# Optimization experiments

Measured on AMD Instinct MI355X. Metric: run time of the kernel, lower is better.

The kernel has to match this reference:

```python
import jax, jax.numpy as jnp
import numpy as np

B, T, M, P, N2 = 16, 8192, 128, 128, 128  # N2 = N//2 complex modes

def setup_inputs() -> dict:
    key = jax.random.key(0)
    k1, k2, k3, k4, k5 = jax.random.split(key, 5)
    u = jax.random.normal(k1, (B, T, M), dtype=jnp.float32)
    # log-parametrized Lambda (S5 'log' convention): Lambda = -exp(row0) + 1j*row1
    log_re = jnp.log(jax.random.uniform(k2, (N2,), minval=0.1, maxval=1.0))
    im = jnp.pi * jnp.arange(N2, dtype=jnp.float32)  # HiPPO-like imaginary spread
    Lambda_param = jnp.stack([log_re, im], axis=0).astype(jnp.float32)
    B_param = jax.random.normal(k3, (2, N2, M), dtype=jnp.float32) / np.sqrt(M)
    C_param = jax.random.normal(k4, (2, P, N2), dtype=jnp.float32) / np.sqrt(N2)
    delta = jnp.array([0.01], dtype=jnp.float32)  # default_\u0394
    return {"u": u, "Lambda_param": Lambda_param, "B_param": B_param,
            "C_param": C_param, "delta": delta}

def reference(u, Lambda_param, B_param, C_param, delta):
    # Reconstruct complex continuous-time matrices
    Lam = (-jnp.exp(Lambda_param[0]) + 1j * Lambda_param[1]).astype(jnp.complex64)   # (N2,)
    Bc = (B_param[0] + 1j * B_param[1]).astype(jnp.complex64)                        # (N2, M)
    Cc = (C_param[0] + 1j * C_param[1]).astype(jnp.complex64)                        # (P, N2)
    d = delta[0]
    # ZOH discretization: Lambda_d = exp(Lam*d), Bd = ((Lambda_d - 1)/Lam) * B
    Ld = jnp.exp(Lam * d)                                                            # (N2,)
    Bd = ((Ld - 1.0) / Lam)[:, None] * Bc                                            # (N2, M)
    # Input projection: Bu[b,t,n] = sum_m u[b,t,m] * Bd[n,m]
    Bu = jnp.einsum('btm,nm->btn', u.astype(jnp.complex64), Bd)                      # (B,T,N2)
    # Parallel scan of x_{k+1} = Ld * x_k + Bu_k, x_0 = 0 -> x holds x_1..x_T
    A = jnp.broadcast_to(Ld, Bu.shape)
    def comb(e1, e2):
        a1, b1 = e1
        a2, b2 = e2
        return (a1 * a2, a2 * b1 + b2)
    _, x = jax.lax.associative_scan(comb, (A, Bu), axis=1)                           # (B,T,N2)
    # return_next_y=True: y_k = 2*Re(C x_{k+1})
    y = 2.0 * jnp.real(jnp.einsum('btn,pn->btp', x, Cc))                             # (B,T,P)
    return y
```

## Files before the change

### kernel.cpp

```cpp
#include <hip/hip_runtime.h>
#include <hip/hip_bf16.h>

#define LCH 128
#define NCH 64
#define NCHUNKS 1024

typedef __attribute__((ext_vector_type(8))) short short8v;
typedef __attribute__((ext_vector_type(4))) short short4v;
typedef __attribute__((ext_vector_type(4))) float f32x4;

#define W2_LDINV 0
#define W2_LDP   16384
#define W2_E     32768
#define W2_CIN   163840
#define WS_WPACK_BYTE  (589824 * 4)
#define WS_CCPACK_BYTE (589824 * 4 + 65536)

#define BUS_BYTE(s, np) ((((s) >> 3) * 4096) + ((np) * 16) + (((s) & 7) * 2))

__device__ inline unsigned short f2bf(float f) {
    union { __hip_bfloat16 h; unsigned short u; } v;
    v.h = __float2bfloat16(f);
    return v.u;
}
__device__ inline short4v pack4(float a, float b, float c, float d) {
    union { __hip_bfloat162 h2[2]; short4v s4; } pk;
    pk.h2[0] = __float22bfloat162_rn(make_float2(a, b));
    pk.h2[1] = __float22bfloat162_rn(make_float2(c, d));
    return pk.s4;
}

__global__ void k0_pows(const float* __restrict__ lp, const float* __restrict__ delta,
                        float2* __restrict__ ws2) {
    const int r = blockIdx.x;
    const int tid = threadIdx.x;
    const int n = tid & 127;
    const double d = (double)delta[0];
    const double lre = -exp((double)lp[n]);
    const double lim = (double)lp[128 + n];
    const double kk = (double)(r + 1) * d;
    if (tid < 128) {
        const double mag = exp(-lre * kk);
        ws2[W2_LDINV + r * 128 + n] = make_float2((float)(mag * cos(lim * kk)),
                                                  (float)(-mag * sin(lim * kk)));
    } else {
        const double mag = exp(lre * kk);
        ws2[W2_LDP + r * 128 + n] = make_float2((float)(mag * cos(lim * kk)),
                                                (float)(mag * sin(lim * kk)));
    }
}

__global__ void k0_wpack(const float* __restrict__ lp, const float* __restrict__ bp,
                         const float* __restrict__ delta, unsigned short* __restrict__ wpack) {
    const int gid = blockIdx.x * 512 + threadIdx.x;
    const int j = gid & 7;
    const int lane = (gid >> 3) & 63;
    const int ks = (gid >> 9) & 3;
    const int ntile = gid >> 11;
    const int np = ntile * 16 + (lane & 15);
    const int m = ks * 32 + ((lane >> 4) & 3) * 8 + j;
    const int n = np & 127;
    const double d = (double)delta[0];
    const double lre = -exp((double)lp[n]);
    const double lim = (double)lp[128 + n];
    const double er = exp(lre * d);
    const double ldr = er * cos(lim * d), ldi = er * sin(lim * d);
    const double nr = ldr - 1.0, ni = ldi;
    const double den = lre * lre + lim * lim;
    const double cr = (nr * lre + ni * lim) / den;
    const double ci = (ni * lre - nr * lim) / den;
    const double br = (double)bp[n * 128 + m];
    const double bi = (double)bp[16384 + n * 128 + m];
    const double v = (np < 128) ? (cr * br - ci * bi) : (cr * bi + ci * br);
    wpack[gid] = f2bf((float)v);
}

__global__ void k0_cpack(const float* __restrict__ cp, unsigned short* __restrict__ ccpack) {
    const int gid = blockIdx.x * 512 + threadIdx.x;
    const int j = gid & 7;
    const int lane = (gid >> 3) & 63;
    const int ks = (gid >> 9) & 7;
    const int ptile = gid >> 12;
    const int p = ptile * 16 + (lane & 15);
    const int k = ks * 32 + ((lane >> 4) & 3) * 8 + j;
    const int n = k >> 1;
    const float v = ((k & 1) == 0) ? 2.0f * cp[p * 128 + n] : -2.0f * cp[16384 + p * 128 + n];
    ccpack[gid] = f2bf(v);
}

__device__ inline void stage_u(const float* __restrict__ uchunk, unsigned short* lds_u) {
    const float4* uf = (const float4*)uchunk;
    const int tid = threadIdx.x;
#pragma unroll
    for (int it = 0; it < 8; ++it) {
        const int f4 = it * 512 + tid;
        const float4 v = uf[f4];
        const int t = f4 >> 5;
        const int m = (f4 & 31) * 4;
        const int byte = (t * 256 + m * 2) ^ ((t & 7) << 4);
        *(short4v*)((char*)lds_u + byte) = pack4(v.x, v.y, v.z, v.w);
    }
}

__global__ __launch_bounds__(512, 4) void k1_end(const float* __restrict__ u,
                                                 float2* __restrict__ ws2,
                                                 const unsigned short* __restrict__ wpack) {
    __shared__ unsigned short lds_u[16384];
    const int tid = threadIdx.x;
    const int lane = tid & 63;
    const int w = tid >> 6;
    const int tl = lane & 15;
    const int gq = (lane >> 4) & 3;
    const int g = blockIdx.x;
    const int b = g >> 6;
    const int c = g & 63;
    const int n = w * 16 + tl;
    stage_u(u + (size_t)(b * 8192 + c * 128) * 128, lds_u);
    __syncthreads();
    const short8v* wp = (const short8v*)wpack;
    float er = 0.f, ei = 0.f;
#pragma unroll
    for (int h = 0; h < 2; ++h) {
        f32x4 acc[4][2];
#pragma unroll
        for (int i = 0; i < 4; ++i) { acc[i][0] = (f32x4)0.f; acc[i][1] = (f32x4)0.f; }
        __builtin_amdgcn_s_setprio(1);
#pragma unroll
        for (int ks = 0; ks < 4; ++ks) {
            const short8v b0 = wp[(w * 4 + ks) * 64 + lane];
            const short8v b1 = wp[((8 + w) * 4 + ks) * 64 + lane];
#pragma unroll
            for (int tt2 = 0; tt2 < 4; ++tt2) {
                const int t = (h * 4 + tt2) * 16 + tl;
                const int byte = (t * 256 + (ks * 32 + gq * 8) * 2) ^ ((t & 7) << 4);
                const short8v a = *(const short8v*)((const char*)lds_u + byte);
                acc[tt2][0] = __builtin_amdgcn_mfma_f32_16x16x32_bf16(a, b0, acc[tt2][0], 0, 0, 0);
                acc[tt2][1] = __builtin_amdgcn_mfma_f32_16x16x32_bf16(a, b1, acc[tt2][1], 0, 0, 0);
            }
        }
        __builtin_amdgcn_s_setprio(0);
        __builtin_amdgcn_sched_barrier(0);
#pragma unroll
        for (int tt2 = 0; tt2 < 4; ++tt2) {
#pragma unroll
            for (int reg = 0; reg < 4; ++reg) {
                const int r = (h * 4 + tt2) * 16 + gq * 4 + reg;
                const float2 li = ws2[W2_LDINV + r * 128 + n];
                const float br = acc[tt2][0][reg], bi = acc[tt2][1][reg];
                er += li.x * br - li.y * bi;
                ei += li.x * bi + li.y * br;
            }
        }
        __builtin_amdgcn_sched_barrier(0);
    }
    er += __shfl_xor(er, 16); ei += __shfl_xor(ei, 16);
    er += __shfl_xor(er, 32); ei += __shfl_xor(ei, 32);
    const float2 ld = ws2[W2_LDP + 127 * 128 + n];
    if (lane < 16) {
        ws2[W2_E + g * 128 + n] = make_float2(ld.x * er - ld.y * ei,
                                              ld.x * ei + ld.y * er);
    }
}

__global__ void k2_carry(float2* __restrict__ ws2) {
    const int idx = blockIdx.x * 256 + threadIdx.x;
    const int b = idx >> 7;
    const int n = idx & 127;
    const float2 l = ws2[W2_LDP + 127 * 128 + n];
    float cr = 0.f, ci = 0.f;
    for (int c = 0; c < NCH; ++c) {
        const int o = (b * NCH + c) * 128 + n;
        ws2[W2_CIN + o] = make_float2(cr, ci);
        const float2 e = ws2[W2_E + o];
        const float nr = fmaf(l.x, cr, fmaf(-l.y, ci, e.x));
        const float ni = fmaf(l.x, ci, fmaf(l.y, cr, e.y));
        cr = nr; ci = ni;
    }
}

__global__ __launch_bounds__(512, 4) void k3_main(const float* __restrict__ u,
                                                  const float2* __restrict__ ws2,
                                                  const unsigned short* __restrict__ wpack,
                                                  const unsigned short* __restrict__ ccpack,
                                                  float* __restrict__ y) {
    __shared__ unsigned short lds[32768];
    unsigned short* lds_u = lds;
    const int tid = threadIdx.x;
    const int lane = tid & 63;
    const int w = tid >> 6;
    const int tl = lane & 15;
    const int gq = (lane >> 4) & 3;
    const int g = blockIdx.x;
    const int b = g >> 6;
    const int c = g & 63;
    const int n = w * 16 + tl;

    stage_u(u + (size_t)(b * 8192 + c * 128) * 128, lds_u);
    __syncthreads();

    const short8v* wp = (const short8v*)wpack;
#pragma unroll
    for (int hh = 0; hh < 2; ++hh) {
        const int h = 1 - hh;
        f32x4 acc[4][2];
#pragma unroll
        for (int i = 0; i < 4; ++i) { acc[i][0] = (f32x4)0.f; acc[i][1] = (f32x4)0.f; }
        __builtin_amdgcn_s_setprio(1);
#pragma unroll
        for (int ks = 0; ks < 4; ++ks) {
            const short8v b0 = wp[(w * 4 + ks) * 64 + lane];
            const short8v b1 = wp[((8 + w) * 4 + ks) * 64 + lane];
#pragma unroll
            for (int tt2 = 0; tt2 < 4; ++tt2) {
                const int t = (h * 4 + tt2) * 16 + tl;
                const int byte = (t * 256 + (ks * 32 + gq * 8) * 2) ^ ((t & 7) << 4);
                const short8v a = *(const short8v*)((const char*)lds_u + byte);
                acc[tt2][0] = __builtin_amdgcn_mfma_f32_16x16x32_bf16(a, b0, acc[tt2][0], 0, 0, 0);
                acc[tt2][1] = __builtin_amdgcn_mfma_f32_16x16x32_bf16(a, b1, acc[tt2][1], 0, 0, 0);
            }
        }
        __builtin_amdgcn_s_setprio(0);
        __builtin_amdgcn_sched_barrier(0);
        if (h == 0) __syncthreads();
#pragma unroll
        for (int tt2 = 0; tt2 < 4; ++tt2) {
            float vr[4], vi[4];
#pragma unroll
            for (int reg = 0; reg < 4; ++reg) {
                const int r = (h * 4 + tt2) * 16 + gq * 4 + reg;
                const float2 li = ws2[W2_LDINV + r * 128 + n];
                const float br = acc[tt2][0][reg], bi = acc[tt2][1][reg];
                vr[reg] = li.x * br - li.y * bi;
                vi[reg] = li.x * bi + li.y * br;
            }
            const int s0 = (h * 4 + tt2) * 16 + gq * 4;
            const int rowr = w * 16 + tl;
            const int rowi = 128 + rowr;
            *(short4v*)((char*)lds + BUS_BYTE(s0, rowr)) = pack4(vr[0], vr[1], vr[2], vr[3]);
            *(short4v*)((char*)lds + BUS_BYTE(s0, rowi)) = pack4(vi[0], vi[1], vi[2], vi[3]);
        }
        __builtin_amdgcn_sched_barrier(0);
    }

    short8v ONES, D0, D1;
#pragma unroll
    for (int j = 0; j < 8; ++j) {
        const int sl = gq * 8 + j;
        ONES[j] = (short)0x3F80;
        D0[j] = (sl <= tl) ? (short)0x3F80 : (short)0;
        D1[j] = (sl <= tl + 16) ? (short)0x3F80 : (short)0;
    }
    f32x4 z[8][2];
#pragma unroll
    for (int i = 0; i < 8; ++i) { z[i][0] = (f32x4)0.f; z[i][1] = (f32x4)0.f; }
#pragma unroll
    for (int ks = 0; ks < 4; ++ks) {
        const int sb = ks * 32 + gq * 8;
        const int rowr = w * 16 + tl;
        const int rowi = 128 + rowr;
        const short8v b0 = *(const short8v*)((const char*)lds + BUS_BYTE(sb, rowr));
        const short8v b1 = *(const short8v*)((const char*)lds + BUS_BYTE(sb, rowi));
#pragma unroll
        for (int tt = 0; tt < 8; ++tt) {
            if (tt < 2 * ks) continue;
            const short8v a = (tt == 2 * ks) ? D0 : ((tt == 2 * ks + 1) ? D1 : ONES);
            z[tt][0] = __builtin_amdgcn_mfma_f32_16x16x32_bf16(a, b0, z[tt][0], 0, 0, 0);
            z[tt][1] = __builtin_amdgcn_mfma_f32_16x16x32_bf16(a, b1, z[tt][1], 0, 0, 0);
        }
    }
    __syncthreads();

    const float2 cin = ws2[W2_CIN + g * 128 + n];
#pragma unroll
    for (int tt = 0; tt < 8; ++tt) {
#pragma unroll
        for (int reg = 0; reg < 4; ++reg) {
            const int r = tt * 16 + gq * 4 + reg;
            const float2 ld = ws2[W2_LDP + r * 128 + n];
            const float zr = z[tt][0][reg] + cin.x;
            const float zi = z[tt][1][reg] + cin.y;
            const float xr = ld.x * zr - ld.y * zi;
            const float xi = ld.x * zi + ld.y * zr;
            union { __hip_bfloat162 h2; unsigned uu; } pk;
            pk.h2 = __float22bfloat162_rn(make_float2(xr, xi));
            const int byte = (r * 512 + n * 4) ^ ((r & 7) << 4);
            *(unsigned*)((char*)lds + byte) = pk.uu;
        }
    }
    __syncthreads();

    const short8v* cc = (const short8v*)ccpack;
    f32x4 yac[8];
#pragma unroll
    for (int i = 0; i < 8; ++i) yac[i] = (f32x4)0.f;
    __builtin_amdgcn_s_setprio(1);
#pragma unroll
    for (int ks = 0; ks < 8; ++ks) {
        const short8v bfrg = cc[(w * 8 + ks) * 64 + lane];
#pragma unroll
        for (int tt = 0; tt < 8; ++tt) {
            const int t = tt * 16 + tl;
            const int byte = (t * 512 + (ks * 32 + gq * 8) * 2) ^ ((t & 7) << 4);
            const short8v a = *(const short8v*)((const char*)lds + byte);
            yac[tt] = __builtin_amdgcn_mfma_f32_16x16x32_bf16(a, bfrg, yac[tt], 0, 0, 0);
        }
    }
    __builtin_amdgcn_s_setprio(0);
    const int p = w * 16 + tl;
    float* yrow = y + (size_t)(b * 8192 + c * 128) * 128;
#pragma unroll
    for (int tt = 0; tt < 8; ++tt) {
#pragma unroll
        for (int reg = 0; reg < 4; ++reg) {
            const int t = tt * 16 + gq * 4 + reg;
            yrow[t * 128 + p] = yac[tt][reg];
        }
    }
}

extern "C" void kernel_launch(void* const* d_in, const int* in_sizes, int n_in,
                              void* d_out, int out_size, void* d_ws, size_t ws_size,
                              hipStream_t stream) {
    const float* u     = (const float*)d_in[0];
    const float* lp    = (const float*)d_in[1];
    const float* bp    = (const float*)d_in[2];
    const float* cp    = (const float*)d_in[3];
    const float* delta = (const float*)d_in[4];
    float* y  = (float*)d_out;
    float2* ws2 = (float2*)d_ws;
    unsigned short* wpack  = (unsigned short*)((char*)d_ws + WS_WPACK_BYTE);
    unsigned short* ccpack = (unsigned short*)((char*)d_ws + WS_CCPACK_BYTE);

    k0_pows <<<128, 256, 0, stream>>>(lp, delta, ws2);
    k0_wpack<<<64, 512, 0, stream>>>(lp, bp, delta, wpack);
    k0_cpack<<<64, 512, 0, stream>>>(cp, ccpack);
    k1_end  <<<NCHUNKS, 512, 0, stream>>>(u, ws2, wpack);
    k2_carry<<<8, 256, 0, stream>>>(ws2);
    k3_main <<<NCHUNKS, 512, 0, stream>>>(u, ws2, wpack, ccpack, y);
}
```

Before: 88.36 us.

## Materialize bf16 Bu to global workspace instead of recomputing input projection

The first pass now stores the Lambda-inverse-scaled Bu chunk (bf16, 64KB per chunk) to global workspace while it computes the chunk end-state sums. The final pass reads that buffer back instead of re-staging u and redoing the input-projection MFMAs. This removes a second read of u and a repeat of the projection GEMM, at the cost of writing and reading 64MB of intermediate data. The new path is taken only when the workspace is large enough, otherwise the old three-kernel path runs.

```diff
diff --git a/kernel.cpp b/kernel.cpp
--- a/kernel.cpp
+++ b/kernel.cpp
@@ -13,8 +13,10 @@
 #define W2_LDP   16384
 #define W2_E     32768
 #define W2_CIN   163840
-#define WS_WPACK_BYTE  (589824 * 4)
-#define WS_CCPACK_BYTE (589824 * 4 + 65536)
+#define WS_WPACK_BYTE  2359296
+#define WS_CCPACK_BYTE (2359296 + 65536)
+#define WS_BUS_BYTE    (2359296 + 131072)
+#define WS_NEED ((size_t)WS_BUS_BYTE + (size_t)NCHUNKS * 65536)
 
 #define BUS_BYTE(s, np) ((((s) >> 3) * 4096) + ((np) * 16) + (((s) & 7) * 2))
 
@@ -102,6 +104,185 @@
     }
 }
 
+__global__ __launch_bounds__(512, 6) void k3a_bus(const float* __restrict__ u,
+                                                  float2* __restrict__ ws2,
+                                                  const unsigned short* __restrict__ wpack,
+                                                  char* __restrict__ busg) {
+    __shared__ unsigned short lds_u[16384];
+    const int tid = threadIdx.x;
+    const int lane = tid & 63;
+    const int w = tid >> 6;
+    const int tl = lane & 15;
+    const int gq = (lane >> 4) & 3;
+    const int g = blockIdx.x;
+    const int b = g >> 6;
+    const int c = g & 63;
+    const int n = w * 16 + tl;
+    const short8v* wp = (const short8v*)wpack;
+    char* busc = busg + (size_t)g * 65536;
+
+    stage_u(u + (size_t)(b * 8192 + c * 128) * 128, lds_u);
+    __syncthreads();
+
+    float er = 0.f, ei = 0.f;
+#pragma unroll
+    for (int h = 0; h < 2; ++h) {
+        f32x4 acc[4][2];
+#pragma unroll
+        for (int i = 0; i < 4; ++i) { acc[i][0] = (f32x4)0.f; acc[i][1] = (f32x4)0.f; }
+        __builtin_amdgcn_s_setprio(1);
+#pragma unroll
+        for (int ks = 0; ks < 4; ++ks) {
+            const short8v b0 = wp[(w * 4 + ks) * 64 + lane];
+            const short8v b1 = wp[((8 + w) * 4 + ks) * 64 + lane];
+#pragma unroll
+            for (int tt2 = 0; tt2 < 4; ++tt2) {
+                const int t = (h * 4 + tt2) * 16 + tl;
+                const int byte = (t * 256 + (ks * 32 + gq * 8) * 2) ^ ((t & 7) << 4);
+                const short8v a = *(const short8v*)((const char*)lds_u + byte);
+                acc[tt2][0] = __builtin_amdgcn_mfma_f32_16x16x32_bf16(a, b0, acc[tt2][0], 0, 0, 0);
+                acc[tt2][1] = __builtin_amdgcn_mfma_f32_16x16x32_bf16(a, b1, acc[tt2][1], 0, 0, 0);
+            }
+        }
+        __builtin_amdgcn_s_setprio(0);
+        __builtin_amdgcn_sched_barrier(0);
+#pragma unroll
+        for (int tt2 = 0; tt2 < 4; ++tt2) {
+            float vr[4], vi[4];
+#pragma unroll
+            for (int reg = 0; reg < 4; ++reg) {
+                const int r = (h * 4 + tt2) * 16 + gq * 4 + reg;
+                const float2 li = ws2[W2_LDINV + r * 128 + n];
+                const float br = acc[tt2][0][reg], bi = acc[tt2][1][reg];
+                vr[reg] = li.x * br - li.y * bi;
+                vi[reg] = li.x * bi + li.y * br;
+                er += vr[reg];
+                ei += vi[reg];
+            }
+            const int s0 = (h * 4 + tt2) * 16 + gq * 4;
+            const int rowr = w * 16 + tl;
+            const int rowi = 128 + rowr;
+            *(short4v*)(busc + BUS_BYTE(s0, rowr)) = pack4(vr[0], vr[1], vr[2], vr[3]);
+            *(short4v*)(busc + BUS_BYTE(s0, rowi)) = pack4(vi[0], vi[1], vi[2], vi[3]);
+        }
+        __builtin_amdgcn_sched_barrier(0);
+    }
+    er += __shfl_xor(er, 16); ei += __shfl_xor(ei, 16);
+    er += __shfl_xor(er, 32); ei += __shfl_xor(ei, 32);
+    const float2 ld = ws2[W2_LDP + 127 * 128 + n];
+    if (lane < 16) {
+        ws2[W2_E + g * 128 + n] = make_float2(ld.x * er - ld.y * ei,
+                                              ld.x * ei + ld.y * er);
+    }
+}
+
+__global__ void k2_carry(float2* __restrict__ ws2) {
+    const int idx = blockIdx.x * 256 + threadIdx.x;
+    const int b = idx >> 7;
+    const int n = idx & 127;
+    const float2 l = ws2[W2_LDP + 127 * 128 + n];
+    float cr = 0.f, ci = 0.f;
+    for (int c = 0; c < NCH; ++c) {
+        const int o = (b * NCH + c) * 128 + n;
+        ws2[W2_CIN + o] = make_float2(cr, ci);
+        const float2 e = ws2[W2_E + o];
+        const float nr = fmaf(l.x, cr, fmaf(-l.y, ci, e.x));
+        const float ni = fmaf(l.x, ci, fmaf(l.y, cr, e.y));
+        cr = nr; ci = ni;
+    }
+}
+
+__global__ __launch_bounds__(512, 4) void k3b_out(const float2* __restrict__ ws2,
+                                                  const char* __restrict__ busg,
+                                                  const unsigned short* __restrict__ ccpack,
+                                                  float* __restrict__ y) {
+    __shared__ unsigned short lds[32768];
+    const int tid = threadIdx.x;
+    const int lane = tid & 63;
+    const int w = tid >> 6;
+    const int tl = lane & 15;
+    const int gq = (lane >> 4) & 3;
+    const int g = blockIdx.x;
+    const int b = g >> 6;
+    const int c = g & 63;
+    const int n = w * 16 + tl;
+    const short8v* cc8 = (const short8v*)ccpack;
+    const char* busc = busg + (size_t)g * 65536;
+
+    short8v ONES, D0, D1;
+#pragma unroll
+    for (int j = 0; j < 8; ++j) {
+        const int sl = gq * 8 + j;
+        ONES[j] = (short)0x3F80;
+        D0[j] = (sl <= tl) ? (short)0x3F80 : (short)0;
+        D1[j] = (sl <= tl + 16) ? (short)0x3F80 : (short)0;
+    }
+    f32x4 z[8][2];
+#pragma unroll
+    for (int i = 0; i < 8; ++i) { z[i][0] = (f32x4)0.f; z[i][1] = (f32x4)0.f; }
+#pragma unroll
+    for (int ks = 0; ks < 4; ++ks) {
+        const int sb = ks * 32 + gq * 8;
+        const int rowr = w * 16 + tl;
+        const int rowi = 128 + rowr;
+        const short8v b0 = *(const short8v*)(busc + BUS_BYTE(sb, rowr));
+        const short8v b1 = *(const short8v*)(busc + BUS_BYTE(sb, rowi));
+#pragma unroll
+        for (int tt = 0; tt < 8; ++tt) {
+            if (tt < 2 * ks) continue;
+            const short8v a = (tt == 2 * ks) ? D0 : ((tt == 2 * ks + 1) ? D1 : ONES);
+            z[tt][0] = __builtin_amdgcn_mfma_f32_16x16x32_bf16(a, b0, z[tt][0], 0, 0, 0);
+            z[tt][1] = __builtin_amdgcn_mfma_f32_16x16x32_bf16(a, b1, z[tt][1], 0, 0, 0);
+        }
+    }
+
+    const float2 cin = ws2[W2_CIN + g * 128 + n];
+#pragma unroll
+    for (int tt = 0; tt < 8; ++tt) {
+#pragma unroll
+        for (int reg = 0; reg < 4; ++reg) {
+            const int r = tt * 16 + gq * 4 + reg;
+            const float2 ld = ws2[W2_LDP + r * 128 + n];
+            const float zr = z[tt][0][reg] + cin.x;
+            const float zi = z[tt][1][reg] + cin.y;
+            const float xr = ld.x * zr - ld.y * zi;
+            const float xi = ld.x * zi + ld.y * zr;
+            union { __hip_bfloat162 h2; unsigned uu; } pk;
+            pk.h2 = __float22bfloat162_rn(make_float2(xr, xi));
+            const int byte = (r * 512 + n * 4) ^ ((r & 7) << 4);
+            *(unsigned*)((char*)lds + byte) = pk.uu;
+        }
+    }
+    __syncthreads();
+
+    f32x4 yac[8];
+#pragma unroll
+    for (int i = 0; i < 8; ++i) yac[i] = (f32x4)0.f;
+    __builtin_amdgcn_s_setprio(1);
+#pragma unroll
+    for (int ks = 0; ks < 8; ++ks) {
+        const short8v bfrg = cc8[(w * 8 + ks) * 64 + lane];
+#pragma unroll
+        for (int tt = 0; tt < 8; ++tt) {
+            const int t = tt * 16 + tl;
+            const int byte = (t * 512 + (ks * 32 + gq * 8) * 2) ^ ((t & 7) << 4);
+            const short8v a = *(const short8v*)((const char*)lds + byte);
+            yac[tt] = __builtin_amdgcn_mfma_f32_16x16x32_bf16(a, bfrg, yac[tt], 0, 0, 0);
+        }
+    }
+    __builtin_amdgcn_s_setprio(0);
+    const int p = w * 16 + tl;
+    float* yrow = y + (size_t)(b * 8192 + c * 128) * 128;
+#pragma unroll
+    for (int tt = 0; tt < 8; ++tt) {
+#pragma unroll
+        for (int reg = 0; reg < 4; ++reg) {
+            const int t = tt * 16 + gq * 4 + reg;
+            yrow[t * 128 + p] = yac[tt][reg];
+        }
+    }
+}
+
 __global__ __launch_bounds__(512, 4) void k1_end(const float* __restrict__ u,
                                                  float2* __restrict__ ws2,
                                                  const unsigned short* __restrict__ wpack) {
@@ -162,29 +343,12 @@
     }
 }
 
-__global__ void k2_carry(float2* __restrict__ ws2) {
-    const int idx = blockIdx.x * 256 + threadIdx.x;
-    const int b = idx >> 7;
-    const int n = idx & 127;
-    const float2 l = ws2[W2_LDP + 127 * 128 + n];
-    float cr = 0.f, ci = 0.f;
-    for (int c = 0; c < NCH; ++c) {
-        const int o = (b * NCH + c) * 128 + n;
-        ws2[W2_CIN + o] = make_float2(cr, ci);
-        const float2 e = ws2[W2_E + o];
-        const float nr = fmaf(l.x, cr, fmaf(-l.y, ci, e.x));
-        const float ni = fmaf(l.x, ci, fmaf(l.y, cr, e.y));
-        cr = nr; ci = ni;
-    }
-}
-
 __global__ __launch_bounds__(512, 4) void k3_main(const float* __restrict__ u,
                                                   const float2* __restrict__ ws2,
                                                   const unsigned short* __restrict__ wpack,
                                                   const unsigned short* __restrict__ ccpack,
                                                   float* __restrict__ y) {
     __shared__ unsigned short lds[32768];
-    unsigned short* lds_u = lds;
     const int tid = threadIdx.x;
     const int lane = tid & 63;
     const int w = tid >> 6;
@@ -194,11 +358,11 @@
     const int b = g >> 6;
     const int c = g & 63;
     const int n = w * 16 + tl;
-
-    stage_u(u + (size_t)(b * 8192 + c * 128) * 128, lds_u);
+    const short8v* wp = (const short8v*)wpack;
+    const short8v* cc8 = (const short8v*)ccpack;
+
+    stage_u(u + (size_t)(b * 8192 + c * 128) * 128, lds);
     __syncthreads();
-
-    const short8v* wp = (const short8v*)wpack;
 #pragma unroll
     for (int hh = 0; hh < 2; ++hh) {
         const int h = 1 - hh;
@@ -214,7 +378,7 @@
             for (int tt2 = 0; tt2 < 4; ++tt2) {
                 const int t = (h * 4 + tt2) * 16 + tl;
                 const int byte = (t * 256 + (ks * 32 + gq * 8) * 2) ^ ((t & 7) << 4);
-                const short8v a = *(const short8v*)((const char*)lds_u + byte);
+                const short8v a = *(const short8v*)((const char*)lds + byte);
                 acc[tt2][0] = __builtin_amdgcn_mfma_f32_16x16x32_bf16(a, b0, acc[tt2][0], 0, 0, 0);
                 acc[tt2][1] = __builtin_amdgcn_mfma_f32_16x16x32_bf16(a, b1, acc[tt2][1], 0, 0, 0);
             }
@@ -241,7 +405,6 @@
         }
         __builtin_amdgcn_sched_barrier(0);
     }
-
     short8v ONES, D0, D1;
 #pragma unroll
     for (int j = 0; j < 8; ++j) {
@@ -269,7 +432,6 @@
         }
     }
     __syncthreads();
-
     const float2 cin = ws2[W2_CIN + g * 128 + n];
 #pragma unroll
     for (int tt = 0; tt < 8; ++tt) {
@@ -288,15 +450,13 @@
         }
     }
     __syncthreads();
-
-    const short8v* cc = (const short8v*)ccpack;
     f32x4 yac[8];
 #pragma unroll
     for (int i = 0; i < 8; ++i) yac[i] = (f32x4)0.f;
     __builtin_amdgcn_s_setprio(1);
 #pragma unroll
     for (int ks = 0; ks < 8; ++ks) {
-        const short8v bfrg = cc[(w * 8 + ks) * 64 + lane];
+        const short8v bfrg = cc8[(w * 8 + ks) * 64 + lane];
 #pragma unroll
         for (int tt = 0; tt < 8; ++tt) {
             const int t = tt * 16 + tl;
@@ -330,11 +490,19 @@
     float2* ws2 = (float2*)d_ws;
     unsigned short* wpack  = (unsigned short*)((char*)d_ws + WS_WPACK_BYTE);
     unsigned short* ccpack = (unsigned short*)((char*)d_ws + WS_CCPACK_BYTE);
+    char* busg = (char*)d_ws + WS_BUS_BYTE;
 
     k0_pows <<<128, 256, 0, stream>>>(lp, delta, ws2);
     k0_wpack<<<64, 512, 0, stream>>>(lp, bp, delta, wpack);
     k0_cpack<<<64, 512, 0, stream>>>(cp, ccpack);
-    k1_end  <<<NCHUNKS, 512, 0, stream>>>(u, ws2, wpack);
-    k2_carry<<<8, 256, 0, stream>>>(ws2);
-    k3_main <<<NCHUNKS, 512, 0, stream>>>(u, ws2, wpack, ccpack, y);
-}
+
+    if (ws_size >= WS_NEED) {
+        k3a_bus <<<NCHUNKS, 512, 0, stream>>>(u, ws2, wpack, busg);
+        k2_carry<<<8, 256, 0, stream>>>(ws2);
+        k3b_out <<<NCHUNKS, 512, 0, stream>>>(ws2, busg, ccpack, y);
+    } else {
+        k1_end  <<<NCHUNKS, 512, 0, stream>>>(u, ws2, wpack);
+        k2_carry<<<8, 256, 0, stream>>>(ws2);
+        k3_main <<<NCHUNKS, 512, 0, stream>>>(u, ws2, wpack, ccpack, y);
+    }
+}
```

Result: faster. 84.32 us (-4.6%).
